# Optimization experiments

Measured on AMD Instinct MI355X. Metric: run time of the kernel, lower is better.

## Reference

```python
import jax, jax.numpy as jnp
import numpy as np

B, L, D, H, FD, NL, NV, NN, MAXSPD = 2, 1024, 1024, 16, 512, 4, 5000, 5000, 30
DF = 4 * D
S = L + 2  # 1 graph token + 1 sos token + L data tokens
DH = D // H
NEG = -1e9  # finite stand-in for -inf query mask (constant per softmax row -> same probs, no NaNs)


def rmsnorm(x, w, eps=1e-6):
    return x * jax.lax.rsqrt(jnp.mean(x * x, axis=-1, keepdims=True) + eps) * w


def setup_inputs() -> dict:
    key = jax.random.key(0)
    ks = jax.random.split(key, 24)
    f = lambda k, sh, s=0.02: (jax.random.normal(k, sh, jnp.float32) * s)
    return {
        "graph_features": jax.random.normal(ks[0], (B, 1, D), jnp.float32),
        "input_features": jax.random.normal(ks[1], (B, L, FD), jnp.float32),
        "proj_W": f(ks[2], (FD, D)),
        "proj_b": jnp.zeros((D,), jnp.float32),
        "sos_token": f(ks[3], (1, 1, D)),
        "node_emb": f(ks[4], (NN, D)),
        "type_emb": f(ks[5], (2, D)),
        "pos_emb": f(ks[6], (S, D)),
        "spd_emb": f(ks[7], (MAXSPD + 2, H)),
        "attn_norm_w": jnp.ones((NL, D), jnp.float32),
        "wq": f(ks[8], (NL, D, D)),
        "wk": f(ks[9], (NL, D, D)),
        "wv": f(ks[10], (NL, D, D)),
        "wo": f(ks[11], (NL, D, D)),
        "ffn_norm_w": jnp.ones((NL, D), jnp.float32),
        "w1": f(ks[12], (NL, D, DF)),
        "w2": f(ks[13], (NL, DF, D)),
        "w3": f(ks[14], (NL, D, DF)),
        "final_norm_w": jnp.ones((D,), jnp.float32),
        "out_W": f(ks[15], (D, NV)),
        "out_b": jnp.zeros((NV,), jnp.float32),
        "subnode_ids": jax.random.randint(ks[16], (B, L), 0, NN),
        "token_mask_len": jax.random.randint(ks[17], (B,), 1, L),
        "spd_indices": jax.random.randint(ks[18], (B, L, L), 0, MAXSPD + 1),
        "start_pos": 0,
    }


def reference(graph_features, input_features, proj_W, proj_b, sos_token, node_emb,
              type_emb, pos_emb, spd_emb, attn_norm_w, wq, wk, wv, wo, ffn_norm_w,
              w1, w2, w3, final_norm_w, out_W, out_b,
              subnode_ids, token_mask_len, spd_indices, start_pos):
    bsz = input_features.shape[0]
    glen = graph_features.shape[1]  # 1

    # token embedding fusion
    h_data = input_features @ proj_W + proj_b                      # [B,L,D]
    sos = jnp.broadcast_to(sos_token, (bsz, 1, D))
    h_tokens = jnp.concatenate([sos, h_data], axis=1)              # [B,L+1,D]
    sub_ext = jnp.concatenate([jnp.zeros((bsz, 1), subnode_ids.dtype), subnode_ids], axis=1)
    h_tokens = h_tokens + node_emb[sub_ext] + type_emb[0]
    h_graph = graph_features + type_emb[1]
    h = jnp.concatenate([h_graph, h_tokens], axis=1)               # [B,S,D]
    seqlen = h.shape[1]

    # SPD relative bias -> [B,H,S,S]
    max_spd = spd_emb.shape[0] - 2
    full_spd = jnp.full((bsz, seqlen, seqlen), max_spd + 1, dtype=jnp.int32)
    full_spd = full_spd.at[:, 2:, 2:].set(spd_indices.astype(jnp.int32))
    full_spd = full_spd.at[:, 0, 0].set(0).at[:, 1, 1].set(0)
    graph_bias = jnp.transpose(spd_emb[full_spd], (0, 3, 1, 2))

    h = h + pos_emb[:seqlen]

    # additive query-validity mask [B,1,S,1] broadcast over keys
    positions = jnp.arange(seqlen)[None, :]
    valid = positions < (token_mask_len[:, None] + 1 + glen)
    mask = jnp.where(valid, 0.0, NEG).astype(h.dtype)[:, None, :, None]

    scale = 1.0 / np.sqrt(DH)
    n_heads = graph_bias.shape[1]
    for i in range(wq.shape[0]):
        x = rmsnorm(h, attn_norm_w[i])
        q = (x @ wq[i]).reshape(bsz, seqlen, n_heads, DH)
        k = (x @ wk[i]).reshape(bsz, seqlen, n_heads, DH)
        v = (x @ wv[i]).reshape(bsz, seqlen, n_heads, DH)
        scores = jnp.einsum('bqhd,bkhd->bhqk', q, k) * scale + graph_bias + mask
        p = jax.nn.softmax(scores, axis=-1)
        att = jnp.einsum('bhqk,bkhd->bqhd', p, v).reshape(bsz, seqlen, D) @ wo[i]
        h = h + att
        x2 = rmsnorm(h, ffn_norm_w[i])
        h = h + (jax.nn.silu(x2 @ w1[i]) * (x2 @ w3[i])) @ w2[i]

    h = rmsnorm(h, final_norm_w)
    h_seq = h[:, glen:, :]                                          # [B,L+1,D]
    return (h_seq @ out_W + out_b).astype(jnp.float32)
```

## Files before the change

kernel.cpp:

```cpp
#include <hip/hip_runtime.h>

#define DMODEL 1024
#define DFF    4096
#define NHEAD  16
#define DHEAD  64
#define LTOK   1024
#define SEQ    1026
#define SPAD   1088
#define MPAD   2176
#define NVOC   5000
#define NVOCP  5120
#define MOUT   2050

typedef float  floatx4 __attribute__((ext_vector_type(4)));
typedef __bf16 bf16x8  __attribute__((ext_vector_type(8)));

__device__ __forceinline__ unsigned short f2b(float f) {
  unsigned int u = __builtin_bit_cast(unsigned int, f);
  u += 0x7FFFu + ((u >> 16) & 1u);
  return (unsigned short)(u >> 16);
}
__device__ __forceinline__ float b2f(unsigned short v) {
  return __builtin_bit_cast(float, ((unsigned int)v) << 16);
}
__device__ __forceinline__ void gl2lds16(const void* g, void* l) {
  __builtin_amdgcn_global_load_lds((const __attribute__((address_space(1))) void*)g,
                                   (__attribute__((address_space(3))) void*)l, 16, 0, 0);
}
__device__ __forceinline__ floatx4 mfma16(bf16x8 a, bf16x8 b, floatx4 c) {
  return __builtin_amdgcn_mfma_f32_16x16x32_bf16(a, b, c, 0, 0, 0);
}

__global__ __launch_bounds__(256) void f2b_kernel(const float* __restrict__ s,
                                                  unsigned short* __restrict__ d, int n) {
  int i = (blockIdx.x * 256 + threadIdx.x) * 4;
  if (i >= n) return;
  float4 v = *(const float4*)(s + i);
  ushort4 o; o.x = f2b(v.x); o.y = f2b(v.y); o.z = f2b(v.z); o.w = f2b(v.w);
  *(ushort4*)(d + i) = o;
}

__global__ __launch_bounds__(256) void transconv_kernel(
    const float* __restrict__ p0, const float* __restrict__ p1,
    const float* __restrict__ p2, const float* __restrict__ p3,
    unsigned short* __restrict__ dst, long dstZ, int R, int C) {
  const float* src = (blockIdx.z == 0) ? p0 : (blockIdx.z == 1) ? p1 : (blockIdx.z == 2) ? p2 : p3;
  dst += dstZ * blockIdx.z;
  __shared__ float T[64][68];
  const int r0 = blockIdx.y * 64, c0 = blockIdx.x * 64;
  const int tr = threadIdx.x >> 4, tc = threadIdx.x & 15;
#pragma unroll
  for (int it = 0; it < 4; it++) {
    int rl = tr + it * 16;
    int cg = c0 + tc * 4;
    float4 v = {0.f, 0.f, 0.f, 0.f};
    if (cg < C) v = *(const float4*)(src + (size_t)(r0 + rl) * C + cg);
    T[rl][tc * 4 + 0] = v.x; T[rl][tc * 4 + 1] = v.y;
    T[rl][tc * 4 + 2] = v.z; T[rl][tc * 4 + 3] = v.w;
  }
  __syncthreads();
#pragma unroll
  for (int it = 0; it < 4; it++) {
    int ol = tr + it * 16;
    int oc = c0 + ol;
    if (oc < C) {
      ushort4 o;
      o.x = f2b(T[tc * 4 + 0][ol]); o.y = f2b(T[tc * 4 + 1][ol]);
      o.z = f2b(T[tc * 4 + 2][ol]); o.w = f2b(T[tc * 4 + 3][ol]);
      *(ushort4*)(dst + (size_t)oc * R + r0 + tc * 4) = o;
    }
  }
}

__global__ __launch_bounds__(256) void build_h_kernel(
    float* __restrict__ h, const float* __restrict__ gf, const float* __restrict__ sos,
    const float* __restrict__ nodeE, const float* __restrict__ typeE,
    const float* __restrict__ posE, const int* __restrict__ sub) {
  const int s = blockIdx.x, b = blockIdx.y;
  const int c = threadIdx.x * 4;
  float* o = h + ((size_t)(b * SPAD + s)) * DMODEL + c;
  if (s >= SEQ) { o[0] = 0.f; o[1] = 0.f; o[2] = 0.f; o[3] = 0.f; return; }
  float4 p = *(const float4*)(posE + (size_t)s * DMODEL + c);
  if (s == 0) {
    float4 g = *(const float4*)(gf + (size_t)b * DMODEL + c);
    float4 t = *(const float4*)(typeE + DMODEL + c);
    o[0] = g.x + t.x + p.x; o[1] = g.y + t.y + p.y;
    o[2] = g.z + t.z + p.z; o[3] = g.w + t.w + p.w;
  } else {
    float4 t = *(const float4*)(typeE + c);
    int nid = (s == 1) ? 0 : sub[b * LTOK + s - 2];
    float4 ne = *(const float4*)(nodeE + (size_t)nid * DMODEL + c);
    if (s == 1) {
      float4 ss = *(const float4*)(sos + c);
      o[0] = ss.x + ne.x + t.x + p.x; o[1] = ss.y + ne.y + t.y + p.y;
      o[2] = ss.z + ne.z + t.z + p.z; o[3] = ss.w + ne.w + t.w + p.w;
    } else {
      o[0] += ne.x + t.x + p.x; o[1] += ne.y + t.y + p.y;
      o[2] += ne.z + t.z + p.z; o[3] += ne.w + t.w + p.w;
    }
  }
}

__global__ __launch_bounds__(256) void rmsnorm_kernel(const float* __restrict__ h,
                                                      const float* __restrict__ w,
                                                      unsigned short* __restrict__ out,
                                                      int final_mode) {
  const int r = blockIdx.x;
  int srow = r;
  if (final_mode) {
    if (r >= MOUT) {
      ushort4 z = {0, 0, 0, 0};
      *(ushort4*)(out + (size_t)r * DMODEL + threadIdx.x * 4) = z;
      return;
    }
    int b = r / 1025;
    srow = b * SPAD + 1 + (r - b * 1025);
  }
  float4 x = *(const float4*)(h + (size_t)srow * DMODEL + threadIdx.x * 4);
  float ss = x.x * x.x + x.y * x.y + x.z * x.z + x.w * x.w;
#pragma unroll
  for (int off = 32; off > 0; off >>= 1) ss += __shfl_down(ss, off);
  __shared__ float red[4];
  if ((threadIdx.x & 63) == 0) red[threadIdx.x >> 6] = ss;
  __syncthreads();
  float rs = rsqrtf((red[0] + red[1] + red[2] + red[3]) * (1.f / 1024.f) + 1e-6f);
  float4 ww = *(const float4*)(w + threadIdx.x * 4);
  ushort4 o;
  o.x = f2b(x.x * rs * ww.x); o.y = f2b(x.y * rs * ww.y);
  o.z = f2b(x.z * rs * ww.z); o.w = f2b(x.w * rs * ww.w);
  *(ushort4*)(out + (size_t)r * DMODEL + threadIdx.x * 4) = o;
}

__global__ __launch_bounds__(256) void vtrans_kernel(const unsigned short* __restrict__ v,
                                                     unsigned short* __restrict__ vt) {
  const int st = blockIdx.x, hh = blockIdx.y, b = blockIdx.z;
  __shared__ unsigned short T[64][72];
  const int tr = threadIdx.x >> 4, tc = threadIdx.x & 15;
#pragma unroll
  for (int it = 0; it < 4; it++) {
    int r = tr + it * 16;
    ushort4 val = *(const ushort4*)(v + ((size_t)(b * SPAD + st * 64 + r)) * DMODEL + hh * DHEAD + tc * 4);
    T[r][tc * 4 + 0] = val.x; T[r][tc * 4 + 1] = val.y;
    T[r][tc * 4 + 2] = val.z; T[r][tc * 4 + 3] = val.w;
  }
  __syncthreads();
#pragma unroll
  for (int it = 0; it < 4; it++) {
    int d = tr + it * 16;
    ushort4 o;
    o.x = T[tc * 4 + 0][d]; o.y = T[tc * 4 + 1][d];
    o.z = T[tc * 4 + 2][d]; o.w = T[tc * 4 + 3][d];
    *(ushort4*)(vt + (((size_t)(b * NHEAD + hh)) * DHEAD + d) * SPAD + st * 64 + tc * 4) = o;
  }
}

#define PST 80
__global__ __launch_bounds__(256) void attn_kernel(
    const unsigned short* __restrict__ qb, const unsigned short* __restrict__ kb,
    const unsigned short* __restrict__ vt, unsigned short* __restrict__ attb,
    const float* __restrict__ spdE, const int* __restrict__ spd,
    const int* __restrict__ tml) {
  const int qt = blockIdx.x, hh = blockIdx.y, bb = blockIdx.z;
  const int tid = threadIdx.x;
  const int w = tid >> 6, lane = tid & 63;
  const int quad = lane >> 4, l16 = lane & 15;

  __shared__ unsigned short Qs[64 * PST];
  __shared__ unsigned short Ks[64 * PST];
  __shared__ unsigned short Vts[64 * PST];
  __shared__ unsigned short Ps[4 * 16 * PST];
  __shared__ float bias_tab[32];

  if (tid < 32) bias_tab[tid] = spdE[tid * NHEAD + hh];

#pragma unroll
  for (int jj = 0; jj < 2; jj++) {
    int c = tid + (jj << 8);
    int r = c >> 3, ch = c & 7;
    int4 val = *(const int4*)(qb + ((size_t)(bb * SPAD + qt * 64 + r)) * DMODEL + hh * DHEAD + ch * 8);
    *(int4*)(Qs + r * PST + ch * 8) = val;
  }
  const int tmlb = tml[bb];
  __syncthreads();

  bf16x8 aq[2];
  aq[0] = *(const bf16x8*)(Qs + (w * 16 + l16) * PST + quad * 8);
  aq[1] = *(const bf16x8*)(Qs + (w * 16 + l16) * PST + 32 + quad * 8);

  floatx4 O[4];
  float m_i[4], l_i[4];
#pragma unroll
  for (int d = 0; d < 4; d++) { floatx4 z = {0.f, 0.f, 0.f, 0.f}; O[d] = z; }
#pragma unroll
  for (int r = 0; r < 4; r++) { m_i[r] = -3.0e38f; l_i[r] = 0.f; }

  unsigned short* PsW = Ps + w * 16 * PST;

  for (int kt = 0; kt < 17; kt++) {
#pragma unroll
    for (int jj = 0; jj < 2; jj++) {
      int c = tid + (jj << 8);
      int r = c >> 3, ch = c & 7;
      int4 kv = *(const int4*)(kb + ((size_t)(bb * SPAD + kt * 64 + r)) * DMODEL + hh * DHEAD + ch * 8);
      *(int4*)(Ks + r * PST + ch * 8) = kv;
      int4 vv = *(const int4*)(vt + (((size_t)(bb * NHEAD + hh)) * DHEAD + r) * SPAD + kt * 64 + ch * 8);
      *(int4*)(Vts + r * PST + ch * 8) = vv;
    }
    __syncthreads();

    float sc[4][4];
#pragma unroll
    for (int ns = 0; ns < 4; ns++) {
      bf16x8 bk0 = *(const bf16x8*)(Ks + (ns * 16 + l16) * PST + quad * 8);
      bf16x8 bk1 = *(const bf16x8*)(Ks + (ns * 16 + l16) * PST + 32 + quad * 8);
      floatx4 c4 = {0.f, 0.f, 0.f, 0.f};
      c4 = mfma16(aq[0], bk0, c4);
      c4 = mfma16(aq[1], bk1, c4);
#pragma unroll
      for (int r = 0; r < 4; r++) sc[ns][r] = c4[r];
    }

#pragma unroll
    for (int r = 0; r < 4; r++) {
      int qg = qt * 64 + w * 16 + quad * 4 + r;
      float maskv = (qg < tmlb + 2) ? 0.f : -1.0e9f;
      int qs = (qg >= 2) ? ((qg - 2 < LTOK) ? qg - 2 : LTOK - 1) : 0;
#pragma unroll
      for (int ns = 0; ns < 4; ns++) {
        int kg = kt * 64 + ns * 16 + l16;
        float sv;
        if (kg >= SEQ) {
          sv = -3.0e38f;
        } else {
          int idx;
          if (qg >= 2 && kg >= 2) {
            idx = spd[((size_t)bb * LTOK + qs) * LTOK + (kg - 2)];
            idx = idx < 0 ? 0 : (idx > 31 ? 31 : idx);
          } else {
            idx = (qg == kg) ? 0 : 31;
          }
          sv = sc[ns][r] * 0.125f + bias_tab[idx] + maskv;
        }
        sc[ns][r] = sv;
      }
    }

    float alpha[4];
#pragma unroll
    for (int r = 0; r < 4; r++) {
      float mx = fmaxf(fmaxf(sc[0][r], sc[1][r]), fmaxf(sc[2][r], sc[3][r]));
#pragma unroll
      for (int off = 1; off < 16; off <<= 1) mx = fmaxf(mx, __shfl_xor(mx, off));
      float mn = fmaxf(m_i[r], mx);
      alpha[r] = __expf(m_i[r] - mn);
      m_i[r] = mn;
      float rs = 0.f;
#pragma unroll
      for (int ns = 0; ns < 4; ns++) { float p = __expf(sc[ns][r] - mn); sc[ns][r] = p; rs += p; }
#pragma unroll
      for (int off = 1; off < 16; off <<= 1) rs += __shfl_xor(rs, off);
      l_i[r] = l_i[r] * alpha[r] + rs;
    }

#pragma unroll
    for (int ns = 0; ns < 4; ns++)
#pragma unroll
      for (int r = 0; r < 4; r++)
        PsW[(quad * 4 + r) * PST + ns * 16 + l16] = f2b(sc[ns][r]);

#pragma unroll
    for (int d = 0; d < 4; d++)
#pragma unroll
      for (int r = 0; r < 4; r++) O[d][r] *= alpha[r];

    bf16x8 ap0 = *(const bf16x8*)(PsW + l16 * PST + quad * 8);
    bf16x8 ap1 = *(const bf16x8*)(PsW + l16 * PST + 32 + quad * 8);
#pragma unroll
    for (int d = 0; d < 4; d++) {
      bf16x8 bv0 = *(const bf16x8*)(Vts + (d * 16 + l16) * PST + quad * 8);
      bf16x8 bv1 = *(const bf16x8*)(Vts + (d * 16 + l16) * PST + 32 + quad * 8);
      O[d] = mfma16(ap0, bv0, O[d]);
      O[d] = mfma16(ap1, bv1, O[d]);
    }
    __syncthreads();
  }

#pragma unroll
  for (int r = 0; r < 4; r++) {
    int qg = qt * 64 + w * 16 + quad * 4 + r;
    float inv = 1.0f / l_i[r];
#pragma unroll
    for (int d = 0; d < 4; d++)
      attb[((size_t)(bb * SPAD + qg)) * DMODEL + hh * DHEAD + d * 16 + l16] = f2b(O[d][r] * inv);
  }
}

__global__ __launch_bounds__(256) void silumul_kernel(const unsigned short* __restrict__ u,
                                                      unsigned short* __restrict__ g, int n) {
  int i = (blockIdx.x * 256 + threadIdx.x) * 4;
  if (i >= n) return;
  const unsigned short* u3 = u + n;
  ushort4 a = *(const ushort4*)(u + i);
  ushort4 c = *(const ushort4*)(u3 + i);
  ushort4 o;
  float x, y;
  x = b2f(a.x); y = b2f(c.x); o.x = f2b(x / (1.f + __expf(-x)) * y);
  x = b2f(a.y); y = b2f(c.y); o.y = f2b(x / (1.f + __expf(-x)) * y);
  x = b2f(a.z); y = b2f(c.z); o.z = f2b(x / (1.f + __expf(-x)) * y);
  x = b2f(a.w); y = b2f(c.w); o.w = f2b(x / (1.f + __expf(-x)) * y);
  *(ushort4*)(g + i) = o;
}

enum { EPI_BF16 = 0, EPI_RESID = 1, EPI_PROJ = 2, EPI_OUT = 3 };

template <int EPI>
__global__ __launch_bounds__(256) void gemm_bt_kernel(
    const unsigned short* __restrict__ A, const unsigned short* __restrict__ Bt,
    void* __restrict__ Cv, const float* __restrict__ bias,
    int M, int N, int K, long zA, long zB, long zC, int Mreal, int Nreal) {
  A += zA * blockIdx.z;
  Bt += zB * blockIdx.z;
  char* Cb = (char*)Cv + zC * blockIdx.z;

  const int tid = threadIdx.x;
  const int lane = tid & 63, wave = tid >> 6;
  const int quad = lane >> 4, l16 = lane & 15;
  const int wr = wave >> 1, wc = wave & 1;
  const int m0 = blockIdx.y << 7, n0 = blockIdx.x << 7;

  __shared__ unsigned short As[128 * 32];
  __shared__ unsigned short Bs[128 * 32];

  floatx4 acc[4][4];
  {
    floatx4 z = {0.f, 0.f, 0.f, 0.f};
#pragma unroll
    for (int i = 0; i < 4; i++)
#pragma unroll
      for (int j = 0; j < 4; j++) acc[i][j] = z;
  }

  for (int k0 = 0; k0 < K; k0 += 32) {
#pragma unroll
    for (int jj = 0; jj < 2; jj++) {
      int c = tid + (jj << 8);
      int r = c >> 2, kc = c & 3;
      gl2lds16(A + (size_t)(m0 + r) * K + k0 + kc * 8, As + c * 8);
      gl2lds16(Bt + (size_t)(n0 + r) * K + k0 + kc * 8, Bs + c * 8);
    }
    __syncthreads();
    bf16x8 a[4], b[4];
#pragma unroll
    for (int i = 0; i < 4; i++) a[i] = *(const bf16x8*)(As + (wr * 64 + i * 16 + l16) * 32 + quad * 8);
#pragma unroll
    for (int j = 0; j < 4; j++) b[j] = *(const bf16x8*)(Bs + (wc * 64 + j * 16 + l16) * 32 + quad * 8);
#pragma unroll
    for (int i = 0; i < 4; i++)
#pragma unroll
      for (int j = 0; j < 4; j++) acc[i][j] = mfma16(a[i], b[j], acc[i][j]);
    __syncthreads();
  }

#pragma unroll
  for (int i = 0; i < 4; i++) {
    const int rb = m0 + wr * 64 + i * 16 + quad * 4;
#pragma unroll
    for (int j = 0; j < 4; j++) {
      const int col = n0 + wc * 64 + j * 16 + l16;
#pragma unroll
      for (int r = 0; r < 4; r++) {
        const int row = rb + r;
        float v = acc[i][j][r];
        if constexpr (EPI == EPI_BF16) {
          ((unsigned short*)Cb)[(size_t)row * N + col] = f2b(v);
        } else if constexpr (EPI == EPI_RESID) {
          float* C = (float*)Cb;
          C[(size_t)row * N + col] += v;
        } else if constexpr (EPI == EPI_PROJ) {
          float* C = (float*)Cb;
          int rr = (row >> 10) * SPAD + 2 + (row & 1023);
          C[(size_t)rr * N + col] = v + bias[col];
        } else {
          if (row < Mreal && col < Nreal)
            ((float*)Cb)[(size_t)row * Nreal + col] = v + bias[col];
        }
      }
    }
  }
}

extern "C" void kernel_launch(void* const* d_in, const int* in_sizes, int n_in,
                              void* d_out, int out_size, void* d_ws, size_t ws_size,
                              hipStream_t stream) {
  const float* gf    = (const float*)d_in[0];
  const float* inpf  = (const float*)d_in[1];
  const float* projW = (const float*)d_in[2];
  const float* projB = (const float*)d_in[3];
  const float* sos   = (const float*)d_in[4];
  const float* nodeE = (const float*)d_in[5];
  const float* typeE = (const float*)d_in[6];
  const float* posE  = (const float*)d_in[7];
  const float* spdE  = (const float*)d_in[8];
  const float* attnW = (const float*)d_in[9];
  const float* wq    = (const float*)d_in[10];
  const float* wk    = (const float*)d_in[11];
  const float* wv    = (const float*)d_in[12];
  const float* wo    = (const float*)d_in[13];
  const float* ffnW  = (const float*)d_in[14];
  const float* w1    = (const float*)d_in[15];
  const float* w2    = (const float*)d_in[16];
  const float* w3    = (const float*)d_in[17];
  const float* finW  = (const float*)d_in[18];
  const float* outW  = (const float*)d_in[19];
  const float* outB  = (const float*)d_in[20];
  const int*   sub   = (const int*)d_in[21];
  const int*   tml   = (const int*)d_in[22];
  const int*   spd   = (const int*)d_in[23];
  float* out = (float*)d_out;
  (void)in_sizes; (void)n_in; (void)out_size; (void)ws_size;

  char* ws = (char*)d_ws;
  constexpr size_t OFF_H     = 0;
  constexpr size_t OFF_XB    = 8912896;
  constexpr size_t OFF_Q     = 13369344;
  constexpr size_t OFF_K     = 17825792;
  constexpr size_t OFF_V     = 22282240;
  constexpr size_t OFF_VT    = 26738688;
  constexpr size_t OFF_ATT   = 31195136;
  constexpr size_t OFF_U     = 35651584;
  constexpr size_t OFF_G     = 71303168;
  constexpr size_t OFF_XF    = 89128960;
  constexpr size_t OFF_INB   = 93585408;
  constexpr size_t OFF_PROJT = 95682560;
  constexpr size_t OFF_OUTWT = 96731136;
  constexpr size_t OFF_SLAB  = 107216896;

  float*          h    = (float*)(ws + OFF_H);
  unsigned short* xb   = (unsigned short*)(ws + OFF_XB);
  unsigned short* qbuf = (unsigned short*)(ws + OFF_Q);
  unsigned short* kbuf = (unsigned short*)(ws + OFF_K);
  unsigned short* vbuf = (unsigned short*)(ws + OFF_V);
  unsigned short* vtb  = (unsigned short*)(ws + OFF_VT);
  unsigned short* attb = (unsigned short*)(ws + OFF_ATT);
  unsigned short* ubuf = (unsigned short*)(ws + OFF_U);
  unsigned short* gbuf = (unsigned short*)(ws + OFF_G);
  unsigned short* xf   = (unsigned short*)(ws + OFF_XF);
  unsigned short* inb  = (unsigned short*)(ws + OFF_INB);
  unsigned short* projT = (unsigned short*)(ws + OFF_PROJT);
  unsigned short* outWT = (unsigned short*)(ws + OFF_OUTWT);
  unsigned short* slab  = (unsigned short*)(ws + OFF_SLAB);

  const long DD = (long)DMODEL * DMODEL;
  const long DDF = (long)DMODEL * DFF;
  const long ZC_TOK = (long)MPAD * DMODEL * 2;
  const long ZC_FF  = (long)MPAD * DFF * 2;

  f2b_kernel<<<1024, 256, 0, stream>>>(inpf, inb, 2048 * 512);
  transconv_kernel<<<dim3(16, 8, 1), 256, 0, stream>>>(projW, projW, projW, projW, projT, 0, 512, 1024);
  transconv_kernel<<<dim3(79, 16, 1), 256, 0, stream>>>(outW, outW, outW, outW, outWT, 0, 1024, NVOC);

  gemm_bt_kernel<EPI_PROJ><<<dim3(8, 16, 1), 256, 0, stream>>>(
      inb, projT, h, projB, 2048, 1024, 512, 0, 0, 0, 0, 0);
  build_h_kernel<<<dim3(SPAD, 2), 256, 0, stream>>>(h, gf, sos, nodeE, typeE, posE, sub);

  for (int i = 0; i < 4; i++) {
    transconv_kernel<<<dim3(16, 16, 4), 256, 0, stream>>>(
        wq + (long)i * DD, wk + (long)i * DD, wv + (long)i * DD, wo + (long)i * DD,
        slab, DD, 1024, 1024);
    transconv_kernel<<<dim3(64, 16, 2), 256, 0, stream>>>(
        w1 + (long)i * DDF, w3 + (long)i * DDF, w1, w1,
        slab + 4 * DD, DDF, 1024, 4096);
    transconv_kernel<<<dim3(16, 64, 1), 256, 0, stream>>>(
        w2 + (long)i * DDF, w2, w2, w2,
        slab + 12 * DD, 0, 4096, 1024);

    rmsnorm_kernel<<<MPAD, 256, 0, stream>>>(h, attnW + i * DMODEL, xb, 0);
    gemm_bt_kernel<EPI_BF16><<<dim3(8, 17, 3), 256, 0, stream>>>(
        xb, slab, qbuf, nullptr, MPAD, 1024, 1024, 0, DD, ZC_TOK, 0, 0);
    vtrans_kernel<<<dim3(17, 16, 2), 256, 0, stream>>>(vbuf, vtb);
    attn_kernel<<<dim3(17, 16, 2), 256, 0, stream>>>(qbuf, kbuf, vtb, attb, spdE, spd, tml);
    gemm_bt_kernel<EPI_RESID><<<dim3(8, 17, 1), 256, 0, stream>>>(
        attb, slab + 3 * DD, h, nullptr, MPAD, 1024, 1024, 0, 0, 0, 0, 0);

    rmsnorm_kernel<<<MPAD, 256, 0, stream>>>(h, ffnW + i * DMODEL, xb, 0);
    gemm_bt_kernel<EPI_BF16><<<dim3(32, 17, 2), 256, 0, stream>>>(
        xb, slab + 4 * DD, ubuf, nullptr, MPAD, 4096, 1024, 0, DDF, ZC_FF, 0, 0);
    silumul_kernel<<<8704, 256, 0, stream>>>(ubuf, gbuf, MPAD * DFF);
    gemm_bt_kernel<EPI_RESID><<<dim3(8, 17, 1), 256, 0, stream>>>(
        gbuf, slab + 12 * DD, h, nullptr, MPAD, 1024, 4096, 0, 0, 0, 0, 0);
  }

  rmsnorm_kernel<<<MPAD, 256, 0, stream>>>(h, finW, xf, 1);
  gemm_bt_kernel<EPI_OUT><<<dim3(40, 17, 1), 256, 0, stream>>>(
      xf, outWT, out, outB, MPAD, NVOCP, 1024, 0, 0, 0, MOUT, NVOC);
}
```

Baseline: 1.790 ms.

## Precompute byte bias indices, prefetch K/V tiles, split-K residual GEMMs with atomics

Adds a one-time kernel that turns the int32 SPD indices into a padded uint8 bias-index table, so the attention kernel reads it in coalesced tiles through LDS instead of doing scattered int32 loads with branches per score. The attention loop also register-prefetches the next K/V/index tile while the current one is computed. The wo and w2 residual GEMMs are split along K (2 and 4 ways) and accumulate into h with atomicAdd, giving more blocks for the low-block-count output projections. The costs are extra LDS, atomic traffic, a non-deterministic summation order, and reuse of the xf buffer region to hold the index table.

```diff
diff --git a/kernel.cpp b/kernel.cpp
--- a/kernel.cpp
+++ b/kernel.cpp
@@ -131,6 +131,29 @@
   *(ushort4*)(out + (size_t)r * DMODEL + threadIdx.x * 4) = o;
 }
 
+__global__ __launch_bounds__(320) void bidx_kernel(const int* __restrict__ spd,
+                                                   unsigned char* __restrict__ bidx) {
+  const int qg = blockIdx.x, b = blockIdx.y;
+  const int k0 = threadIdx.x * 4;
+  if (k0 >= SPAD) return;
+  uchar4 o;
+  unsigned char v[4];
+#pragma unroll
+  for (int j = 0; j < 4; j++) {
+    int kg = k0 + j;
+    if (qg >= SEQ || kg >= SEQ) {
+      v[j] = 32;
+    } else if (qg >= 2 && kg >= 2) {
+      int idx = spd[((size_t)b * LTOK + (qg - 2)) * LTOK + (kg - 2)];
+      v[j] = (unsigned char)(idx < 0 ? 0 : (idx > 31 ? 31 : idx));
+    } else {
+      v[j] = (qg == kg) ? 0 : 31;
+    }
+  }
+  o.x = v[0]; o.y = v[1]; o.z = v[2]; o.w = v[3];
+  *(uchar4*)(bidx + ((size_t)b * SPAD + qg) * SPAD + k0) = o;
+}
+
 __global__ __launch_bounds__(256) void vtrans_kernel(const unsigned short* __restrict__ v,
                                                      unsigned short* __restrict__ vt) {
   const int st = blockIdx.x, hh = blockIdx.y, b = blockIdx.z;
@@ -158,7 +181,7 @@
 __global__ __launch_bounds__(256) void attn_kernel(
     const unsigned short* __restrict__ qb, const unsigned short* __restrict__ kb,
     const unsigned short* __restrict__ vt, unsigned short* __restrict__ attb,
-    const float* __restrict__ spdE, const int* __restrict__ spd,
+    const float* __restrict__ spdE, const unsigned char* __restrict__ bidx,
     const int* __restrict__ tml) {
   const int qt = blockIdx.x, hh = blockIdx.y, bb = blockIdx.z;
   const int tid = threadIdx.x;
@@ -169,9 +192,10 @@
   __shared__ unsigned short Ks[64 * PST];
   __shared__ unsigned short Vts[64 * PST];
   __shared__ unsigned short Ps[4 * 16 * PST];
-  __shared__ float bias_tab[32];
-
-  if (tid < 32) bias_tab[tid] = spdE[tid * NHEAD + hh];
+  __shared__ unsigned char Is[64 * 64];
+  __shared__ float bias_tab[33];
+
+  if (tid < 33) bias_tab[tid] = (tid < 32) ? spdE[tid * NHEAD + hh] : -3.0e38f;
 
 #pragma unroll
   for (int jj = 0; jj < 2; jj++) {
@@ -181,6 +205,20 @@
     *(int4*)(Qs + r * PST + ch * 8) = val;
   }
   const int tmlb = tml[bb];
+
+  const int sr = tid >> 3, sch = tid & 7;
+  const int ir = tid >> 2, ic = (tid & 3) * 16;
+  int4 kreg[2], vreg[2], ireg;
+  {
+    const int kt = 0;
+#pragma unroll
+    for (int jj = 0; jj < 2; jj++) {
+      int r = sr + jj * 32;
+      kreg[jj] = *(const int4*)(kb + ((size_t)(bb * SPAD + kt * 64 + r)) * DMODEL + hh * DHEAD + sch * 8);
+      vreg[jj] = *(const int4*)(vt + (((size_t)(bb * NHEAD + hh)) * DHEAD + r) * SPAD + kt * 64 + sch * 8);
+    }
+    ireg = *(const int4*)(bidx + ((size_t)bb * SPAD + qt * 64 + ir) * SPAD + kt * 64 + ic);
+  }
   __syncthreads();
 
   bf16x8 aq[2];
@@ -195,18 +233,33 @@
   for (int r = 0; r < 4; r++) { m_i[r] = -3.0e38f; l_i[r] = 0.f; }
 
   unsigned short* PsW = Ps + w * 16 * PST;
+  float maskv[4];
+#pragma unroll
+  for (int r = 0; r < 4; r++) {
+    int qg = qt * 64 + w * 16 + quad * 4 + r;
+    maskv[r] = (qg < tmlb + 2) ? 0.f : -1.0e9f;
+  }
 
   for (int kt = 0; kt < 17; kt++) {
 #pragma unroll
     for (int jj = 0; jj < 2; jj++) {
-      int c = tid + (jj << 8);
-      int r = c >> 3, ch = c & 7;
-      int4 kv = *(const int4*)(kb + ((size_t)(bb * SPAD + kt * 64 + r)) * DMODEL + hh * DHEAD + ch * 8);
-      *(int4*)(Ks + r * PST + ch * 8) = kv;
-      int4 vv = *(const int4*)(vt + (((size_t)(bb * NHEAD + hh)) * DHEAD + r) * SPAD + kt * 64 + ch * 8);
-      *(int4*)(Vts + r * PST + ch * 8) = vv;
-    }
+      int r = sr + jj * 32;
+      *(int4*)(Ks + r * PST + sch * 8) = kreg[jj];
+      *(int4*)(Vts + r * PST + sch * 8) = vreg[jj];
+    }
+    *(int4*)(Is + ir * 64 + ic) = ireg;
     __syncthreads();
+
+    if (kt < 16) {
+      const int kn = kt + 1;
+#pragma unroll
+      for (int jj = 0; jj < 2; jj++) {
+        int r = sr + jj * 32;
+        kreg[jj] = *(const int4*)(kb + ((size_t)(bb * SPAD + kn * 64 + r)) * DMODEL + hh * DHEAD + sch * 8);
+        vreg[jj] = *(const int4*)(vt + (((size_t)(bb * NHEAD + hh)) * DHEAD + r) * SPAD + kn * 64 + sch * 8);
+      }
+      ireg = *(const int4*)(bidx + ((size_t)bb * SPAD + qt * 64 + ir) * SPAD + kn * 64 + ic);
+    }
 
     float sc[4][4];
 #pragma unroll
@@ -222,26 +275,11 @@
 
 #pragma unroll
     for (int r = 0; r < 4; r++) {
-      int qg = qt * 64 + w * 16 + quad * 4 + r;
-      float maskv = (qg < tmlb + 2) ? 0.f : -1.0e9f;
-      int qs = (qg >= 2) ? ((qg - 2 < LTOK) ? qg - 2 : LTOK - 1) : 0;
+      const unsigned char* isrow = Is + (w * 16 + quad * 4 + r) * 64;
 #pragma unroll
       for (int ns = 0; ns < 4; ns++) {
-        int kg = kt * 64 + ns * 16 + l16;
-        float sv;
-        if (kg >= SEQ) {
-          sv = -3.0e38f;
-        } else {
-          int idx;
-          if (qg >= 2 && kg >= 2) {
-            idx = spd[((size_t)bb * LTOK + qs) * LTOK + (kg - 2)];
-            idx = idx < 0 ? 0 : (idx > 31 ? 31 : idx);
-          } else {
-            idx = (qg == kg) ? 0 : 31;
-          }
-          sv = sc[ns][r] * 0.125f + bias_tab[idx] + maskv;
-        }
-        sc[ns][r] = sv;
+        int idx = isrow[ns * 16 + l16];
+        sc[ns][r] = sc[ns][r] * 0.125f + bias_tab[idx] + maskv[r];
       }
     }
 
@@ -311,13 +349,13 @@
   *(ushort4*)(g + i) = o;
 }
 
-enum { EPI_BF16 = 0, EPI_RESID = 1, EPI_PROJ = 2, EPI_OUT = 3 };
+enum { EPI_BF16 = 0, EPI_RESID = 1, EPI_PROJ = 2, EPI_OUT = 3, EPI_ATOMIC = 4 };
 
 template <int EPI>
 __global__ __launch_bounds__(256) void gemm_bt_kernel(
     const unsigned short* __restrict__ A, const unsigned short* __restrict__ Bt,
     void* __restrict__ Cv, const float* __restrict__ bias,
-    int M, int N, int K, long zA, long zB, long zC, int Mreal, int Nreal) {
+    int M, int N, int K, int ld, long zA, long zB, long zC, int Mreal, int Nreal) {
   A += zA * blockIdx.z;
   Bt += zB * blockIdx.z;
   char* Cb = (char*)Cv + zC * blockIdx.z;
@@ -345,8 +383,8 @@
     for (int jj = 0; jj < 2; jj++) {
       int c = tid + (jj << 8);
       int r = c >> 2, kc = c & 3;
-      gl2lds16(A + (size_t)(m0 + r) * K + k0 + kc * 8, As + c * 8);
-      gl2lds16(Bt + (size_t)(n0 + r) * K + k0 + kc * 8, Bs + c * 8);
+      gl2lds16(A + (size_t)(m0 + r) * ld + k0 + kc * 8, As + c * 8);
+      gl2lds16(Bt + (size_t)(n0 + r) * ld + k0 + kc * 8, Bs + c * 8);
     }
     __syncthreads();
     bf16x8 a[4], b[4];
@@ -380,6 +418,8 @@
           float* C = (float*)Cb;
           int rr = (row >> 10) * SPAD + 2 + (row & 1023);
           C[(size_t)rr * N + col] = v + bias[col];
+        } else if constexpr (EPI == EPI_ATOMIC) {
+          atomicAdd(&((float*)Cb)[(size_t)row * N + col], v);
         } else {
           if (row < Mreal && col < Nreal)
             ((float*)Cb)[(size_t)row * Nreal + col] = v + bias[col];
@@ -445,6 +485,7 @@
   unsigned short* ubuf = (unsigned short*)(ws + OFF_U);
   unsigned short* gbuf = (unsigned short*)(ws + OFF_G);
   unsigned short* xf   = (unsigned short*)(ws + OFF_XF);
+  unsigned char*  bidx = (unsigned char*)(ws + OFF_XF);
   unsigned short* inb  = (unsigned short*)(ws + OFF_INB);
   unsigned short* projT = (unsigned short*)(ws + OFF_PROJT);
   unsigned short* outWT = (unsigned short*)(ws + OFF_OUTWT);
@@ -458,9 +499,10 @@
   f2b_kernel<<<1024, 256, 0, stream>>>(inpf, inb, 2048 * 512);
   transconv_kernel<<<dim3(16, 8, 1), 256, 0, stream>>>(projW, projW, projW, projW, projT, 0, 512, 1024);
   transconv_kernel<<<dim3(79, 16, 1), 256, 0, stream>>>(outW, outW, outW, outW, outWT, 0, 1024, NVOC);
+  bidx_kernel<<<dim3(SPAD, 2), 320, 0, stream>>>(spd, bidx);
 
   gemm_bt_kernel<EPI_PROJ><<<dim3(8, 16, 1), 256, 0, stream>>>(
-      inb, projT, h, projB, 2048, 1024, 512, 0, 0, 0, 0, 0);
+      inb, projT, h, projB, 2048, 1024, 512, 512, 0, 0, 0, 0, 0);
   build_h_kernel<<<dim3(SPAD, 2), 256, 0, stream>>>(h, gf, sos, nodeE, typeE, posE, sub);
 
   for (int i = 0; i < 4; i++) {
@@ -476,21 +518,21 @@
 
     rmsnorm_kernel<<<MPAD, 256, 0, stream>>>(h, attnW + i * DMODEL, xb, 0);
     gemm_bt_kernel<EPI_BF16><<<dim3(8, 17, 3), 256, 0, stream>>>(
-        xb, slab, qbuf, nullptr, MPAD, 1024, 1024, 0, DD, ZC_TOK, 0, 0);
+        xb, slab, qbuf, nullptr, MPAD, 1024, 1024, 1024, 0, DD, ZC_TOK, 0, 0);
     vtrans_kernel<<<dim3(17, 16, 2), 256, 0, stream>>>(vbuf, vtb);
-    attn_kernel<<<dim3(17, 16, 2), 256, 0, stream>>>(qbuf, kbuf, vtb, attb, spdE, spd, tml);
-    gemm_bt_kernel<EPI_RESID><<<dim3(8, 17, 1), 256, 0, stream>>>(
-        attb, slab + 3 * DD, h, nullptr, MPAD, 1024, 1024, 0, 0, 0, 0, 0);
+    attn_kernel<<<dim3(17, 16, 2), 256, 0, stream>>>(qbuf, kbuf, vtb, attb, spdE, bidx, tml);
+    gemm_bt_kernel<EPI_ATOMIC><<<dim3(8, 17, 2), 256, 0, stream>>>(
+        attb, slab + 3 * DD, h, nullptr, MPAD, 1024, 512, 1024, 512, 512, 0, 0, 0);
 
     rmsnorm_kernel<<<MPAD, 256, 0, stream>>>(h, ffnW + i * DMODEL, xb, 0);
     gemm_bt_kernel<EPI_BF16><<<dim3(32, 17, 2), 256, 0, stream>>>(
-        xb, slab + 4 * DD, ubuf, nullptr, MPAD, 4096, 1024, 0, DDF, ZC_FF, 0, 0);
+        xb, slab + 4 * DD, ubuf, nullptr, MPAD, 4096, 1024, 1024, 0, DDF, ZC_FF, 0, 0);
     silumul_kernel<<<8704, 256, 0, stream>>>(ubuf, gbuf, MPAD * DFF);
-    gemm_bt_kernel<EPI_RESID><<<dim3(8, 17, 1), 256, 0, stream>>>(
-        gbuf, slab + 12 * DD, h, nullptr, MPAD, 1024, 4096, 0, 0, 0, 0, 0);
+    gemm_bt_kernel<EPI_ATOMIC><<<dim3(8, 17, 4), 256, 0, stream>>>(
+        gbuf, slab + 12 * DD, h, nullptr, MPAD, 1024, 1024, 4096, 1024, 1024, 0, 0, 0);
   }
 
   rmsnorm_kernel<<<MPAD, 256, 0, stream>>>(h, finW, xf, 1);
   gemm_bt_kernel<EPI_OUT><<<dim3(40, 17, 1), 256, 0, stream>>>(
-      xf, outWT, out, outB, MPAD, NVOCP, 1024, 0, 0, 0, MOUT, NVOC);
-}
+      xf, outWT, out, outB, MPAD, NVOCP, 1024, 1024, 0, 0, 0, MOUT, NVOC);
+}
```

Result: faster. 1.598 ms (-10.7%).
